# Kernel tuning notes

Measured on AMD Instinct MI355X. Metric: run time of the kernel, lower is better.

The kernel has to match this reference:

```python
import jax, jax.numpy as jnp
import numpy as np

TAU = 0.07
MARGIN = 0.2
NUM_SPECIES = 64  # matches fill_max of species_ids


def _l2norm(x):
    return x / jnp.linalg.norm(x, axis=-1, keepdims=True)


def setup_inputs() -> dict:
    key = jax.random.key(0)
    k1, k2, k3 = jax.random.split(key, 3)
    B, D = 8192, 256
    species_embed = _l2norm(jax.random.normal(k1, (B, D), dtype=jnp.float32))
    text_embed = _l2norm(jax.random.normal(k2, (B, D), dtype=jnp.float32))
    species_ids = jax.random.randint(k3, (B,), 0, NUM_SPECIES, dtype=jnp.int32)
    return {"species_embed": species_embed, "text_embed": text_embed,
            "species_ids": species_ids}


def reference(species_embed, text_embed, species_ids):
    B = species_embed.shape[0]
    dtype = species_embed.dtype

    sim = species_embed @ text_embed.T                      # (B, B)
    same = species_ids[:, None] == species_ids[None, :]     # (B, B) bool, symmetric
    diag_sim = jnp.diagonal(sim)                            # (B,)

    # ---- intra-species symmetric InfoNCE (per-species CE, averaged over species)
    logits = sim / TAU
    neg_inf = jnp.finfo(dtype).min
    masked = jnp.where(same, logits, neg_inf)               # restrict to same-species cols
    diag_logit = diag_sim / TAU
    ce_v2t = jax.scipy.special.logsumexp(masked, axis=1) - diag_logit   # per-row CE
    ce_t2v = jax.scipy.special.logsumexp(masked.T, axis=1) - diag_logit # transpose: same mask is symmetric

    ones = jnp.ones((B,), dtype=dtype)
    counts = jax.ops.segment_sum(ones, species_ids, num_segments=NUM_SPECIES)          # group sizes
    seg_v2t = jax.ops.segment_sum(ce_v2t, species_ids, num_segments=NUM_SPECIES)
    seg_t2v = jax.ops.segment_sum(ce_t2v, species_ids, num_segments=NUM_SPECIES)
    valid_s = counts >= 2                                   # groups with <2 members skipped
    per_species = (seg_v2t + seg_t2v) / (2.0 * jnp.maximum(counts, 1.0))
    n_valid = jnp.maximum(jnp.sum(valid_s.astype(dtype)), 1.0)
    loss_infonce = jnp.sum(jnp.where(valid_s, per_species, 0.0)) / n_valid

    # ---- cross-species triplet (pos = mean same-species sim excl. self, neg = mean diff-species sim)
    same_f = same.astype(dtype)
    row_same_sum = jnp.sum(sim * same_f, axis=1)            # includes diagonal
    row_sum = jnp.sum(sim, axis=1)
    pos_cnt = jnp.sum(same_f, axis=1) - 1.0
    neg_cnt = B - jnp.sum(same_f, axis=1)
    pos_mean = (row_same_sum - diag_sim) / jnp.maximum(pos_cnt, 1.0)
    neg_mean = (row_sum - row_same_sum) / jnp.maximum(neg_cnt, 1.0)
    tri = jax.nn.relu(neg_mean - pos_mean + MARGIN)
    valid_i = (pos_cnt > 0) & (neg_cnt > 0)
    n_valid_i = jnp.maximum(jnp.sum(valid_i.astype(dtype)), 1.0)
    loss_triplet = jnp.sum(jnp.where(valid_i, tri, 0.0)) / n_valid_i

    return loss_infonce + loss_triplet
```

## Files before the change

kernel.cpp:

```cpp
#include <hip/hip_runtime.h>
#include <hip/hip_fp16.h>

#define TAU 0.07f
#define MARGIN 0.2f
#define NSPEC 64
#define BB 8192
#define DD 256

#define WS_SCALARS   0
#define WS_LSEROW    1024
#define WS_LSECOL    33792
#define WS_TS        66560
#define WS_T         132096
#define WS_ZERO_BYTES 133120
#define WS_MEMBER    133120
#define WS_COUNTS    165888
#define WS_OFFSETS   166144

typedef _Float16 half8 __attribute__((ext_vector_type(8)));
typedef float float4v __attribute__((ext_vector_type(4)));
typedef unsigned int uint4v __attribute__((ext_vector_type(4)));

__device__ __forceinline__ uint4v pack8(float4 a, float4 b) {
  half8 h;
  h[0] = (_Float16)a.x; h[1] = (_Float16)a.y; h[2] = (_Float16)a.z; h[3] = (_Float16)a.w;
  h[4] = (_Float16)b.x; h[5] = (_Float16)b.y; h[6] = (_Float16)b.z; h[7] = (_Float16)b.w;
  return __builtin_bit_cast(uint4v, h);
}

__device__ __forceinline__ float dot4(float4 a, float4 b) {
  return a.x * b.x + a.y * b.y + a.z * b.z + a.w * b.w;
}

__global__ void k1_all(const int* __restrict__ ids, int* counts_g, int* offsets_g,
                       int* memberList, float* scalars) {
  __shared__ int cnt[NSPEC];
  __shared__ int off[NSPEC];
  int tid = threadIdx.x;
  if (tid < NSPEC) cnt[tid] = 0;
  __syncthreads();
  int myS[8], myP[8];
  #pragma unroll
  for (int r = 0; r < 8; ++r) {
    int i = r * 1024 + tid;
    int s = ids[i];
    myS[r] = s;
    myP[r] = atomicAdd(&cnt[s], 1);
  }
  __syncthreads();
  if (tid < NSPEC) {
    int o = 0;
    for (int t = 0; t < NSPEC; ++t) o += (t < tid) ? cnt[t] : 0;
    off[tid] = o;
    offsets_g[tid] = o;
    int c = cnt[tid];
    counts_g[tid] = c;
    unsigned long long bv = __ballot(c >= 2);
    float nvi = (c >= 2 && c <= BB - 1) ? (float)c : 0.f;
    for (int o2 = 1; o2 < 64; o2 <<= 1) nvi += __shfl_xor(nvi, o2);
    if (tid == 0) {
      scalars[2] = (float)__popcll(bv);
      scalars[3] = nvi;
    }
  }
  __syncthreads();
  #pragma unroll
  for (int r = 0; r < 8; ++r) {
    int i = r * 1024 + tid;
    memberList[off[myS[r]] + myP[r]] = i;
  }
}

__global__ void kmid(const float* __restrict__ sp, const float* __restrict__ tx,
                     const int* __restrict__ counts, const int* __restrict__ offsets,
                     const int* __restrict__ memberList,
                     float* Ts, float* T, float* lseRow, float* lseCol) {
  __shared__ uint4v frag[1536];
  __shared__ int idx[192];
  int bid = blockIdx.x;
  int tid = threadIdx.x;

  if (bid >= 1024) {
    int r0 = (bid - 1024) * 256;
    int d = tid;
    float acc = 0.f;
    #pragma unroll 8
    for (int rr = 0; rr < 256; ++rr) acc += tx[(r0 + rr) * DD + d];
    atomicAdd(&T[d], acc);
    return;
  }
  if (bid >= 512) {
    int v2 = bid - 512;
    int s = v2 & 63, r = v2 >> 6;
    int m = counts[s], g0 = offsets[s];
    int k0 = (m * r) >> 3, k1e = (m * (r + 1)) >> 3;
    if (k0 >= k1e) return;
    int d = tid;
    float acc = 0.f;
    int k = k0;
    for (; k + 4 <= k1e; k += 4) {
      int i0 = memberList[g0 + k];
      int i1 = memberList[g0 + k + 1];
      int i2 = memberList[g0 + k + 2];
      int i3 = memberList[g0 + k + 3];
      float a0 = tx[i0 * DD + d];
      float a1 = tx[i1 * DD + d];
      float a2 = tx[i2 * DD + d];
      float a3 = tx[i3 * DD + d];
      acc += a0 + a1 + a2 + a3;
    }
    for (; k < k1e; ++k) acc += tx[memberList[g0 + k] * DD + d];
    atomicAdd(&Ts[s * DD + d], acc);
    return;
  }

  int s = bid & 63;
  int m = counts[s];
  int g0 = offsets[s];
  int lane = tid & 63, wv = tid >> 6;
  int quad = lane >> 4, cl = lane & 15;
  int rt0 = (bid >> 6) & 3, ct0 = (bid >> 8) & 1;

  for (int rt = rt0; rt * 64 < m; rt += 4) {
    for (int ct = ct0; ct * 128 < m; ct += 2) {
      __syncthreads();
      if (tid < 192) {
        int base = (tid < 64) ? (rt * 64 + tid) : (ct * 128 + (tid - 64));
        idx[tid] = (base < m) ? memberList[g0 + base] : -1;
      }
      __syncthreads();

      const float* srcB[6];
      bool val[6];
      int dst[6];
      float4 r0[6], r1[6];
      #pragma unroll
      for (int p = 0; p < 6; ++p) {
        int u = p * 256 + tid;
        int isB = u >= 512;
        int v = isB ? (u - 512) : u;
        int row = v >> 3, sub = v & 7;
        int ksl = sub >> 2, q = sub & 3;
        int ridx = idx[isB ? (64 + row) : row];
        val[p] = ridx >= 0;
        srcB[p] = (isB ? tx : sp) + (val[p] ? ridx : 0) * DD + ksl * 32 + q * 8;
        dst[p] = isB ? (512 + (ksl * 128 + row) * 4 + q)
                     : ((ksl * 64 + row) * 4 + q);
      }
      #pragma unroll
      for (int p = 0; p < 6; ++p) {
        r0[p] = *reinterpret_cast<const float4*>(srcB[p]);
        r1[p] = *reinterpret_cast<const float4*>(srcB[p] + 4);
      }

      float4v acc[8];
      #pragma unroll
      for (int cf = 0; cf < 8; ++cf) acc[cf] = (float4v){0.f, 0.f, 0.f, 0.f};

      for (int kc = 0; kc < 4; ++kc) {
        __syncthreads();
        uint4v z4 = (uint4v){0u, 0u, 0u, 0u};
        #pragma unroll
        for (int p = 0; p < 6; ++p)
          frag[dst[p]] = val[p] ? pack8(r0[p], r1[p]) : z4;
        __syncthreads();
        if (kc < 3) {
          #pragma unroll
          for (int p = 0; p < 6; ++p) {
            r0[p] = *reinterpret_cast<const float4*>(srcB[p] + (kc + 1) * 64);
            r1[p] = *reinterpret_cast<const float4*>(srcB[p] + (kc + 1) * 64 + 4);
          }
        }
        #pragma unroll
        for (int ksl = 0; ksl < 2; ++ksl) {
          half8 a = __builtin_bit_cast(half8, frag[(ksl * 64 + wv * 16 + cl) * 4 + quad]);
          #pragma unroll
          for (int cf = 0; cf < 8; ++cf) {
            half8 b = __builtin_bit_cast(half8, frag[512 + (ksl * 128 + cf * 16 + cl) * 4 + quad]);
            acc[cf] = __builtin_amdgcn_mfma_f32_16x16x32_f16(a, b, acc[cf], 0, 0, 0);
          }
        }
      }

      int riBase = rt * 64 + wv * 16 + quad * 4;
      float rowAcc[4] = {0.f, 0.f, 0.f, 0.f};
      #pragma unroll
      for (int cf = 0; cf < 8; ++cf) {
        int ci = ct * 128 + cf * 16 + cl;
        bool cv = ci < m;
        float colAcc = 0.f;
        #pragma unroll
        for (int reg = 0; reg < 4; ++reg) {
          bool rv = (riBase + reg) < m;
          float e = (rv && cv) ? __expf(acc[cf][reg] * (1.f / TAU)) : 0.f;
          rowAcc[reg] += e;
          colAcc += e;
        }
        colAcc += __shfl_xor(colAcc, 16);
        colAcc += __shfl_xor(colAcc, 32);
        if (quad == 0 && cv) atomicAdd(&lseCol[g0 + ci], colAcc);
      }
      #pragma unroll
      for (int reg = 0; reg < 4; ++reg) {
        float v = rowAcc[reg];
        v += __shfl_xor(v, 1);
        v += __shfl_xor(v, 2);
        v += __shfl_xor(v, 4);
        v += __shfl_xor(v, 8);
        if (cl == 0 && (riBase + reg) < m) atomicAdd(&lseRow[g0 + riBase + reg], v);
      }
    }
  }
}

__global__ void kend(const float* __restrict__ sp, const float* __restrict__ tx,
                     const int* __restrict__ ids, const int* __restrict__ counts,
                     const int* __restrict__ memberList,
                     const float* __restrict__ Ts, const float* __restrict__ T,
                     const float* __restrict__ lseRow, const float* __restrict__ lseCol,
                     float* scalars, float* out) {
  __shared__ float red[32];
  int tid = threadIdx.x;
  int gt = blockIdx.x * 1024 + tid;
  int g = gt >> 6, lane = gt & 63;
  int i = memberList[g];
  int s = ids[i];
  int m = counts[s];
  float4 a = *reinterpret_cast<const float4*>(sp + i * DD + lane * 4);
  float4 b = *reinterpret_cast<const float4*>(tx + i * DD + lane * 4);
  float4 c = *reinterpret_cast<const float4*>(Ts + s * DD + lane * 4);
  float4 tv = *reinterpret_cast<const float4*>(T + lane * 4);
  float dDiag = dot4(a, b);
  float dTs   = dot4(a, c);
  float dT    = dot4(a, tv);
  #pragma unroll
  for (int o = 1; o < 64; o <<= 1) {
    dDiag += __shfl_xor(dDiag, o);
    dTs   += __shfl_xor(dTs, o);
    dT    += __shfl_xor(dT, o);
  }
  if (lane == 0) {
    float term = 0.f, tri = 0.f;
    if (m >= 2) {
      term = (__logf(lseRow[g]) + __logf(lseCol[g]) - 2.f * dDiag * (1.f / TAU)) /
             (2.f * (float)m);
      float posMean = (dTs - dDiag) / fmaxf((float)(m - 1), 1.f);
      float negMean = (dT - dTs) / fmaxf((float)(BB - m), 1.f);
      if (m <= BB - 1) tri = fmaxf(negMean - posMean + MARGIN, 0.f);
    }
    int wv = tid >> 6;
    red[wv] = term;
    red[16 + wv] = tri;
  }
  __syncthreads();
  if (tid == 0) {
    float infoS = 0.f, triS = 0.f;
    #pragma unroll
    for (int w = 0; w < 16; ++w) { infoS += red[w]; triS += red[16 + w]; }
    atomicAdd(&scalars[1], infoS);
    atomicAdd(&scalars[0], triS);
    __threadfence();
    unsigned prev = atomicAdd((unsigned*)&scalars[4], 1u);
    if (prev == (unsigned)(gridDim.x - 1)) {
      float fi = atomicAdd(&scalars[1], 0.f);
      float ft = atomicAdd(&scalars[0], 0.f);
      float nv = scalars[2];
      float nvi = scalars[3];
      out[0] = fi / fmaxf(nv, 1.f) + ft / fmaxf(nvi, 1.f);
    }
  }
}

extern "C" void kernel_launch(void* const* d_in, const int* in_sizes, int n_in,
                              void* d_out, int out_size, void* d_ws, size_t ws_size,
                              hipStream_t stream) {
  const float* sp = (const float*)d_in[0];
  const float* tx = (const float*)d_in[1];
  const int* ids = (const int*)d_in[2];
  float* out = (float*)d_out;

  char* ws = (char*)d_ws;
  float* scalars = (float*)(ws + WS_SCALARS);
  float* lseRow = (float*)(ws + WS_LSEROW);
  float* lseCol = (float*)(ws + WS_LSECOL);
  float* Ts = (float*)(ws + WS_TS);
  float* T = (float*)(ws + WS_T);
  int* memberList = (int*)(ws + WS_MEMBER);
  int* counts = (int*)(ws + WS_COUNTS);
  int* offsets = (int*)(ws + WS_OFFSETS);

  hipMemsetAsync(d_ws, 0, WS_ZERO_BYTES, stream);
  k1_all<<<1, 1024, 0, stream>>>(ids, counts, offsets, memberList, scalars);
  kmid<<<1056, 256, 0, stream>>>(sp, tx, counts, offsets, memberList, Ts, T,
                                 lseRow, lseCol);
  kend<<<512, 1024, 0, stream>>>(sp, tx, ids, counts, memberList, Ts, T,
                                 lseRow, lseCol, scalars, out);
}
```

Baseline: 112.0 us.

## Fold workspace zeroing and text column-sum into first kernel, drop memset

Removes the separate hipMemsetAsync. The grouping kernel now runs 33 blocks: block 0 builds counts, offsets and member lists and zeroes the scalars, while blocks 1 to 32 zero the lse/Ts workspace and compute per-chunk partial column sums of the text embeddings. The middle kernel then reduces those 128 partials in a single block instead of having 32 blocks atomically add 256-row sums into a pre-zeroed T. This cuts one stream operation and moves the T reduction off the middle kernel's critical path by overlapping it with grouping. In exchange, the first kernel does more work and the final T reduction becomes one serial 128-step loop.

```diff
diff --git a/kernel.cpp b/kernel.cpp
--- a/kernel.cpp
+++ b/kernel.cpp
@@ -8,14 +8,14 @@
 #define DD 256
 
 #define WS_SCALARS   0
+#define WS_COUNTS    64
+#define WS_OFFSETS   320
 #define WS_LSEROW    1024
 #define WS_LSECOL    33792
 #define WS_TS        66560
 #define WS_T         132096
-#define WS_ZERO_BYTES 133120
 #define WS_MEMBER    133120
-#define WS_COUNTS    165888
-#define WS_OFFSETS   166144
+#define WS_TPART     165888
 
 typedef _Float16 half8 __attribute__((ext_vector_type(8)));
 typedef float float4v __attribute__((ext_vector_type(4)));
@@ -32,61 +32,80 @@
   return a.x * b.x + a.y * b.y + a.z * b.z + a.w * b.w;
 }
 
-__global__ void k1_all(const int* __restrict__ ids, int* counts_g, int* offsets_g,
-                       int* memberList, float* scalars) {
-  __shared__ int cnt[NSPEC];
-  __shared__ int off[NSPEC];
-  int tid = threadIdx.x;
-  if (tid < NSPEC) cnt[tid] = 0;
-  __syncthreads();
-  int myS[8], myP[8];
-  #pragma unroll
-  for (int r = 0; r < 8; ++r) {
-    int i = r * 1024 + tid;
-    int s = ids[i];
-    myS[r] = s;
-    myP[r] = atomicAdd(&cnt[s], 1);
-  }
-  __syncthreads();
-  if (tid < NSPEC) {
-    int o = 0;
-    for (int t = 0; t < NSPEC; ++t) o += (t < tid) ? cnt[t] : 0;
-    off[tid] = o;
-    offsets_g[tid] = o;
-    int c = cnt[tid];
-    counts_g[tid] = c;
-    unsigned long long bv = __ballot(c >= 2);
-    float nvi = (c >= 2 && c <= BB - 1) ? (float)c : 0.f;
-    for (int o2 = 1; o2 < 64; o2 <<= 1) nvi += __shfl_xor(nvi, o2);
-    if (tid == 0) {
-      scalars[2] = (float)__popcll(bv);
-      scalars[3] = nvi;
-    }
-  }
-  __syncthreads();
-  #pragma unroll
-  for (int r = 0; r < 8; ++r) {
-    int i = r * 1024 + tid;
-    memberList[off[myS[r]] + myP[r]] = i;
-  }
-}
-
-__global__ void kmid(const float* __restrict__ sp, const float* __restrict__ tx,
-                     const int* __restrict__ counts, const int* __restrict__ offsets,
-                     const int* __restrict__ memberList,
-                     float* Ts, float* T, float* lseRow, float* lseCol) {
+__global__ void kA(const int* __restrict__ ids, const float* __restrict__ tx,
+                   char* __restrict__ ws) {
+  int bid = blockIdx.x, tid = threadIdx.x;
+  if (bid == 0) {
+    int* counts_g = (int*)(ws + WS_COUNTS);
+    int* offsets_g = (int*)(ws + WS_OFFSETS);
+    int* memberList = (int*)(ws + WS_MEMBER);
+    float* scalars = (float*)(ws + WS_SCALARS);
+    __shared__ int cnt[NSPEC];
+    __shared__ int off[NSPEC];
+    if (tid < 8) ((unsigned*)scalars)[tid] = 0u;
+    if (tid < NSPEC) cnt[tid] = 0;
+    __syncthreads();
+    int myS[8], myP[8];
+    #pragma unroll
+    for (int r = 0; r < 8; ++r) {
+      int i = r * 1024 + tid;
+      int s = ids[i];
+      myS[r] = s;
+      myP[r] = atomicAdd(&cnt[s], 1);
+    }
+    __syncthreads();
+    if (tid < NSPEC) {
+      int o = 0;
+      for (int t = 0; t < NSPEC; ++t) o += (t < tid) ? cnt[t] : 0;
+      off[tid] = o;
+      offsets_g[tid] = o;
+      int c = cnt[tid];
+      counts_g[tid] = c;
+      unsigned long long bv = __ballot(c >= 2);
+      float nvi = (c >= 2 && c <= BB - 1) ? (float)c : 0.f;
+      for (int o2 = 1; o2 < 64; o2 <<= 1) nvi += __shfl_xor(nvi, o2);
+      if (tid == 0) {
+        scalars[2] = (float)__popcll(bv);
+        scalars[3] = nvi;
+      }
+    }
+    __syncthreads();
+    #pragma unroll
+    for (int r = 0; r < 8; ++r) {
+      int i = r * 1024 + tid;
+      memberList[off[myS[r]] + myP[r]] = i;
+    }
+  } else {
+    int b = bid - 1;
+    if (tid < 256) {
+      float4v z4 = {0.f, 0.f, 0.f, 0.f};
+      *(float4v*)(ws + WS_LSEROW + b * 4096 + tid * 16) = z4;
+    }
+    float* Tpart = (float*)(ws + WS_TPART);
+    int d = tid & 255, q = tid >> 8;
+    int row0 = b * 256 + q * 64;
+    float acc = 0.f;
+    #pragma unroll 8
+    for (int rr = 0; rr < 64; ++rr) acc += tx[(row0 + rr) * DD + d];
+    Tpart[(b * 4 + q) * DD + d] = acc;
+  }
+}
+
+__global__ void kB(const float* __restrict__ sp, const float* __restrict__ tx,
+                   const int* __restrict__ counts, const int* __restrict__ offsets,
+                   const int* __restrict__ memberList, const float* __restrict__ Tpart,
+                   float* Ts, float* T, float* lseRow, float* lseCol) {
   __shared__ uint4v frag[1536];
   __shared__ int idx[192];
   int bid = blockIdx.x;
   int tid = threadIdx.x;
 
-  if (bid >= 1024) {
-    int r0 = (bid - 1024) * 256;
+  if (bid == 1024) {
     int d = tid;
     float acc = 0.f;
     #pragma unroll 8
-    for (int rr = 0; rr < 256; ++rr) acc += tx[(r0 + rr) * DD + d];
-    atomicAdd(&T[d], acc);
+    for (int p = 0; p < 128; ++p) acc += Tpart[p * DD + d];
+    T[d] = acc;
     return;
   }
   if (bid >= 512) {
@@ -213,12 +232,12 @@
   }
 }
 
-__global__ void kend(const float* __restrict__ sp, const float* __restrict__ tx,
-                     const int* __restrict__ ids, const int* __restrict__ counts,
-                     const int* __restrict__ memberList,
-                     const float* __restrict__ Ts, const float* __restrict__ T,
-                     const float* __restrict__ lseRow, const float* __restrict__ lseCol,
-                     float* scalars, float* out) {
+__global__ void kC(const float* __restrict__ sp, const float* __restrict__ tx,
+                   const int* __restrict__ ids, const int* __restrict__ counts,
+                   const int* __restrict__ memberList,
+                   const float* __restrict__ Ts, const float* __restrict__ T,
+                   const float* __restrict__ lseRow, const float* __restrict__ lseCol,
+                   float* scalars, float* out) {
   __shared__ float red[32];
   int tid = threadIdx.x;
   int gt = blockIdx.x * 1024 + tid;
@@ -281,18 +300,18 @@
 
   char* ws = (char*)d_ws;
   float* scalars = (float*)(ws + WS_SCALARS);
+  int* counts = (int*)(ws + WS_COUNTS);
+  int* offsets = (int*)(ws + WS_OFFSETS);
   float* lseRow = (float*)(ws + WS_LSEROW);
   float* lseCol = (float*)(ws + WS_LSECOL);
   float* Ts = (float*)(ws + WS_TS);
   float* T = (float*)(ws + WS_T);
   int* memberList = (int*)(ws + WS_MEMBER);
-  int* counts = (int*)(ws + WS_COUNTS);
-  int* offsets = (int*)(ws + WS_OFFSETS);
-
-  hipMemsetAsync(d_ws, 0, WS_ZERO_BYTES, stream);
-  k1_all<<<1, 1024, 0, stream>>>(ids, counts, offsets, memberList, scalars);
-  kmid<<<1056, 256, 0, stream>>>(sp, tx, counts, offsets, memberList, Ts, T,
-                                 lseRow, lseCol);
-  kend<<<512, 1024, 0, stream>>>(sp, tx, ids, counts, memberList, Ts, T,
-                                 lseRow, lseCol, scalars, out);
-}
+  float* Tpart = (float*)(ws + WS_TPART);
+
+  kA<<<33, 1024, 0, stream>>>(ids, tx, ws);
+  kB<<<1025, 256, 0, stream>>>(sp, tx, counts, offsets, memberList, Tpart,
+                               Ts, T, lseRow, lseCol);
+  kC<<<512, 1024, 0, stream>>>(sp, tx, ids, counts, memberList, Ts, T,
+                               lseRow, lseCol, scalars, out);
+}
```

After: 108.6 us (median of 2 runs). 3.0% less time.
